# Performance work log

Hardware: AMD Instinct MI355X
Metric: run time of the kernel (lower is better)

The kernel has to match this reference:

```python
import jax, jax.numpy as jnp
import numpy as np

N_NODE = 100000
N_EDGE = 1600000
IN_DIM = 128
HID = [64, 64]
OUT_DIM = 32
NUM_GRAPHS = 256


def setup_inputs() -> dict:
    key = jax.random.key(0)
    ks = jax.random.split(key, 12)
    x = jax.random.normal(ks[0], (N_NODE, IN_DIM), dtype=jnp.float32)
    senders = jax.random.randint(ks[1], (N_EDGE,), 0, N_NODE, dtype=jnp.int32)
    receivers = jax.random.randint(ks[2], (N_EDGE,), 0, N_NODE, dtype=jnp.int32)
    batch = jnp.sort(jax.random.randint(ks[3], (N_NODE,), 0, NUM_GRAPHS, dtype=jnp.int32))
    # Dense params for the 3 GCN layers (Glorot-ish scaling)
    def dense(k, din, dout):
        return jax.random.normal(k, (din, dout), dtype=jnp.float32) / np.sqrt(din)
    W1 = dense(ks[4], IN_DIM, HID[0]); b1 = jnp.zeros((HID[0],), jnp.float32)
    W2 = dense(ks[5], HID[0], HID[1]); b2 = jnp.zeros((HID[1],), jnp.float32)
    W3 = dense(ks[6], HID[1], OUT_DIM); b3 = jnp.zeros((OUT_DIM,), jnp.float32)
    return {"x": x, "W1": W1, "b1": b1, "W2": W2, "b2": b2, "W3": W3, "b3": b3,
            "senders": senders, "receivers": receivers, "batch": batch,
            "num_graphs": NUM_GRAPHS}


def _gcn_layer(x, W, b, senders, receivers, n_node):
    # Dense transform
    x = x @ W + b  # [N, dout]
    ones = jnp.ones(senders.shape[0], dtype=x.dtype)
    sender_deg = jax.ops.segment_sum(ones, senders, n_node)      # out-degree
    receiver_deg = jax.ops.segment_sum(ones, receivers, n_node)  # in-degree
    # symmetric normalization: D^{-1/2} A D^{-1/2}
    x = x * jax.lax.rsqrt(jnp.maximum(sender_deg, 1.0))[:, None]
    x = jax.ops.segment_sum(x[senders], receivers, n_node)       # gather + scatter-sum
    x = x * jax.lax.rsqrt(jnp.maximum(receiver_deg, 1.0))[:, None]
    return x


def reference(x, W1, b1, W2, b2, W3, b3, senders, receivers, batch, num_graphs):
    n_node = x.shape[0]
    x = jax.nn.relu(_gcn_layer(x, W1, b1, senders, receivers, n_node))
    x = jax.nn.relu(_gcn_layer(x, W2, b2, senders, receivers, n_node))
    x = _gcn_layer(x, W3, b3, senders, receivers, n_node)
    # graph-level sum pooling
    return jax.ops.segment_sum(x, batch, num_graphs)  # [num_graphs, OUT_DIM]
```

## Files before the change

### kernel.cpp

```cpp
#include <hip/hip_runtime.h>
#include <hip/hip_bf16.h>

#define N_NODE   100000
#define N_EDGE   1600000
#define IN_DIM   128
#define HID1     64
#define HID2     64
#define OUT_DIM  32
#define NUM_GRAPHS 256

#define NBUCK    782
#define BBLK     500
#define EPB      3200
#define STAGE_CAP 4096

typedef unsigned int uint;
typedef unsigned char uchar;
typedef unsigned short ushort_t;
typedef short bf16x8 __attribute__((ext_vector_type(8)));
typedef float f32x4 __attribute__((ext_vector_type(4)));

__device__ __forceinline__ float bflo(uint p) { return __uint_as_float(p << 16); }
__device__ __forceinline__ float bfhi(uint p) { return __uint_as_float(p & 0xFFFF0000u); }
__device__ __forceinline__ uint bfpack(float a, float b) {
    uint ua = __float_as_uint(a), ub = __float_as_uint(b);
    ua = (ua + 0x7FFFu + ((ua >> 16) & 1u)) >> 16;
    ub = (ub + 0x7FFFu + ((ub >> 16) & 1u)) & 0xFFFF0000u;
    return ua | ub;
}
__device__ __forceinline__ ushort_t bf16r(float f) {
    uint ua = __float_as_uint(f);
    return (ushort_t)((ua + 0x7FFFu + ((ua >> 16) & 1u)) >> 16);
}


__global__ __launch_bounds__(256)
void k_count(const int2* __restrict__ snd2, const int2* __restrict__ rcv2,
             int* __restrict__ cntRA, int* __restrict__ cntSA) {
    __shared__ int cntR[NBUCK];
    __shared__ int cntS[NBUCK];
    const int t = threadIdx.x, blk = blockIdx.x;
    for (int i = t; i < NBUCK; i += 256) { cntR[i] = 0; cntS[i] = 0; }
    __syncthreads();
    const int base2 = blk * (EPB / 2);
    for (int i = 0; i < 7; ++i) {
        int local2 = i * 256 + t;
        if (local2 < EPB / 2) {
            int2 r = rcv2[base2 + local2];
            int2 s = snd2[base2 + local2];
            atomicAdd(&cntR[r.x >> 7], 1);
            atomicAdd(&cntR[r.y >> 7], 1);
            atomicAdd(&cntS[s.x >> 7], 1);
            atomicAdd(&cntS[s.y >> 7], 1);
        }
    }
    __syncthreads();
    for (int i = t; i < NBUCK; i += 256) {
        cntRA[blk * NBUCK + i] = cntR[i];
        cntSA[blk * NBUCK + i] = cntS[i];
    }
}

__global__ __launch_bounds__(256)
void k_scanb(int* __restrict__ cntRA, int* __restrict__ cntSA,
             int* __restrict__ rTotal, int* __restrict__ sTotal) {
    const int which = blockIdx.x / NBUCK;
    const int b = blockIdx.x % NBUCK;
    int* cntA = which ? cntSA : cntRA;
    int* total = which ? sTotal : rTotal;
    const int t = threadIdx.x, lane = t & 63, wave = t >> 6;
    __shared__ int sW[4];
    int carry = 0;
    for (int k = 0; k < 2; ++k) {
        int idx = k * 256 + t;
        int v = (idx < BBLK) ? cntA[idx * NBUCK + b] : 0;
        int inc = v;
        #pragma unroll
        for (int o = 1; o < 64; o <<= 1) { int n = __shfl_up(inc, o); if (lane >= o) inc += n; }
        if (lane == 63) sW[wave] = inc;
        __syncthreads();
        int wOff = 0;
        for (int w = 0; w < wave; ++w) wOff += sW[w];
        int tot = sW[0] + sW[1] + sW[2] + sW[3];
        int excl = carry + wOff + inc - v;
        if (idx < BBLK) cntA[idx * NBUCK + b] = excl;
        carry += tot;
        __syncthreads();
    }
    if (t == 0) total[b] = carry;
}

__global__ __launch_bounds__(256)
void k_scanB(const int* __restrict__ rTotal, const int* __restrict__ sTotal,
             int* __restrict__ rBase, int* __restrict__ sBase) {
    const int* total = blockIdx.x ? sTotal : rTotal;
    int* base = blockIdx.x ? sBase : rBase;
    const int t = threadIdx.x, lane = t & 63, wave = t >> 6;
    __shared__ int sW[4];
    int carry = 0;
    for (int k = 0; k < 4; ++k) {
        int idx = k * 256 + t;
        int v = (idx < NBUCK) ? total[idx] : 0;
        int inc = v;
        #pragma unroll
        for (int o = 1; o < 64; o <<= 1) { int n = __shfl_up(inc, o); if (lane >= o) inc += n; }
        if (lane == 63) sW[wave] = inc;
        __syncthreads();
        int wOff = 0;
        for (int w = 0; w < wave; ++w) wOff += sW[w];
        int tot = sW[0] + sW[1] + sW[2] + sW[3];
        int excl = carry + wOff + inc - v;
        if (idx < NBUCK) base[idx] = excl;
        carry += tot;
        __syncthreads();
    }
    if (t == 0) base[NBUCK] = carry;
}

__global__ __launch_bounds__(256)
void k_place(const int2* __restrict__ snd2, const int2* __restrict__ rcv2,
             const int* __restrict__ rColOff, const int* __restrict__ sColOff,
             const int* __restrict__ rBase, const int* __restrict__ sBase,
             uint* __restrict__ binned, uchar* __restrict__ sBin) {
    __shared__ int curR[NBUCK];
    __shared__ int curS[NBUCK];
    const int t = threadIdx.x, blk = blockIdx.x;
    for (int i = t; i < NBUCK; i += 256) { curR[i] = 0; curS[i] = 0; }
    __syncthreads();
    const int base2 = blk * (EPB / 2);
    for (int i = 0; i < 7; ++i) {
        int local2 = i * 256 + t;
        if (local2 < EPB / 2) {
            int2 r = rcv2[base2 + local2];
            int2 s = snd2[base2 + local2];
            int b0 = r.x >> 7, b1 = r.y >> 7;
            int l0 = atomicAdd(&curR[b0], 1);
            binned[rBase[b0] + rColOff[blk * NBUCK + b0] + l0] = ((uint)s.x << 7) | (uint)(r.x & 127);
            int l1 = atomicAdd(&curR[b1], 1);
            binned[rBase[b1] + rColOff[blk * NBUCK + b1] + l1] = ((uint)s.y << 7) | (uint)(r.y & 127);
            int c0 = s.x >> 7, c1 = s.y >> 7;
            int m0 = atomicAdd(&curS[c0], 1);
            sBin[sBase[c0] + sColOff[blk * NBUCK + c0] + m0] = (uchar)(s.x & 127);
            int m1 = atomicAdd(&curS[c1], 1);
            sBin[sBase[c1] + sColOff[blk * NBUCK + c1] + m1] = (uchar)(s.y & 127);
        }
    }
}

__global__ __launch_bounds__(256)
void k_local(const uint* __restrict__ binned, const uchar* __restrict__ sBin,
             const int* __restrict__ rBase, const int* __restrict__ sBase,
             int* __restrict__ rowptr, float* __restrict__ normS, float* __restrict__ normR,
             int* __restrict__ sortedSrc) {
    __shared__ uint staged[STAGE_CAP];
    __shared__ int cnt[128], excl[128], cur[128], cntS2[128];
    const int b = blockIdx.x, t = threadIdx.x;
    const int e0 = rBase[b], e1 = rBase[b + 1], m = e1 - e0;
    const int s0 = sBase[b], s1 = sBase[b + 1], ms = s1 - s0;
    if (t < 128) { cnt[t] = 0; cur[t] = 0; cntS2[t] = 0; }
    __syncthreads();
    for (int i = t; i < m; i += 256) {
        uint v = binned[e0 + i];
        if (i < STAGE_CAP) staged[i] = v;
        atomicAdd(&cnt[v & 127u], 1);
    }
    for (int i = t; i < ms; i += 256) {
        atomicAdd(&cntS2[(int)sBin[s0 + i]], 1);
    }
    __syncthreads();
    if (t < 64) {
        int v0 = cnt[t], v1 = cnt[64 + t];
        int i0 = v0;
        #pragma unroll
        for (int o = 1; o < 64; o <<= 1) { int n = __shfl_up(i0, o); if (t >= o) i0 += n; }
        excl[t] = i0 - v0;
        int tot0 = __shfl(i0, 63);
        int i1 = v1;
        #pragma unroll
        for (int o = 1; o < 64; o <<= 1) { int n = __shfl_up(i1, o); if (t >= o) i1 += n; }
        excl[64 + t] = tot0 + i1 - v1;
    }
    __syncthreads();
    if (t < 128) {
        int node = b * 128 + t;
        if (node < N_NODE) {
            rowptr[node] = e0 + excl[t];
            normR[node] = rsqrtf(fmaxf((float)cnt[t], 1.0f));
            normS[node] = rsqrtf(fmaxf((float)cntS2[t], 1.0f));
        }
    }
    if (b == NBUCK - 1 && t == 0) rowptr[N_NODE] = e1;
    for (int i = t; i < m; i += 256) {
        uint v = (i < STAGE_CAP) ? staged[i] : binned[e0 + i];
        int n7 = (int)(v & 127u);
        int lpos = atomicAdd(&cur[n7], 1);
        sortedSrc[e0 + excl[n7] + lpos] = (int)(v >> 7);
    }
}


__global__ __launch_bounds__(256)
void k_prepw(const float* __restrict__ W1, const float* __restrict__ W2,
             const float* __restrict__ W3,
             ushort_t* __restrict__ Wt1, ushort_t* __restrict__ Wt2,
             ushort_t* __restrict__ Wt3) {
    int i = blockIdx.x * 256 + threadIdx.x;
    if (i < 8192) {
        int col = i >> 7, k = i & 127;
        Wt1[i] = bf16r(W1[k * 64 + col]);
    } else if (i < 12288) {
        int j = i - 8192; int col = j >> 6, k = j & 63;
        Wt2[j] = bf16r(W2[k * 64 + col]);
    } else if (i < 14336) {
        int j = i - 12288; int col = j >> 6, k = j & 63;
        Wt3[j] = bf16r(W3[k * 32 + col]);
    }
}


template<int K, int N, bool F32IN>
__global__ __launch_bounds__(256)
void k_mgemm(const void* __restrict__ Xv, const ushort_t* __restrict__ Wt,
             const float* __restrict__ bias, const float* __restrict__ normS,
             uint* __restrict__ Y2) {
    __shared__ uint WL[N * K / 2];
    const int tid = threadIdx.x, wave = tid >> 6, lane = tid & 63;
    const uint* Wg = (const uint*)Wt;
    for (int i = tid; i < N * K / 2; i += 256) {
        int col = i / (K / 2);
        WL[i ^ ((col & 7) << 2)] = Wg[i];
    }
    const int m0 = blockIdx.x * 64 + wave * 16;
    const int arow = m0 + (lane & 15);
    const int asrc = (arow < N_NODE) ? arow : 0;
    const int koff = (lane >> 4) * 8;
    bf16x8 afr[K / 32];
    if (F32IN) {
        const float* Xf = (const float*)Xv + (size_t)asrc * K + koff;
        #pragma unroll
        for (int s = 0; s < K / 32; ++s) {
            float4 u = *(const float4*)(Xf + 32 * s);
            float4 v = *(const float4*)(Xf + 32 * s + 4);
            union { uint u4[4]; bf16x8 v8; } c;
            c.u4[0] = bfpack(u.x, u.y); c.u4[1] = bfpack(u.z, u.w);
            c.u4[2] = bfpack(v.x, v.y); c.u4[3] = bfpack(v.z, v.w);
            afr[s] = c.v8;
        }
    } else {
        const uint* Xp = (const uint*)Xv + (size_t)asrc * (K / 2) + (koff >> 1);
        #pragma unroll
        for (int s = 0; s < K / 32; ++s) {
            uint2 q0 = *(const uint2*)(Xp + 16 * s);
            uint2 q1 = *(const uint2*)(Xp + 16 * s + 2);
            union { uint u4[4]; bf16x8 v8; } c;
            c.u4[0] = q0.x; c.u4[1] = q0.y; c.u4[2] = q1.x; c.u4[3] = q1.y;
            afr[s] = c.v8;
        }
    }
    __syncthreads();
    f32x4 acc[N / 16];
    #pragma unroll
    for (int t = 0; t < N / 16; ++t) acc[t] = (f32x4){0.f, 0.f, 0.f, 0.f};
    #pragma unroll
    for (int s = 0; s < K / 32; ++s) {
        #pragma unroll
        for (int t = 0; t < N / 16; ++t) {
            int col = t * 16 + (lane & 15);
            int word = (col * (K / 2) + s * 16 + (koff >> 1)) ^ ((col & 7) << 2);
            bf16x8 bfr = *(const bf16x8*)&WL[word];
            acc[t] = __builtin_amdgcn_mfma_f32_16x16x32_bf16(afr[s], bfr, acc[t], 0, 0, 0);
        }
    }
    const int r0 = m0 + (lane >> 4) * 4;
    float ns[4];
    #pragma unroll
    for (int i = 0; i < 4; ++i) ns[i] = (r0 + i < N_NODE) ? normS[r0 + i] : 0.f;
    #pragma unroll
    for (int t = 0; t < N / 16; ++t) {
        int col = t * 16 + (lane & 15);
        float bv = bias[col];
        #pragma unroll
        for (int i = 0; i < 4; ++i) {
            float v = (acc[t][i] + bv) * ns[i];
            float w = __shfl_down(v, 1);
            if ((lane & 1) == 0 && r0 + i < N_NODE)
                Y2[(size_t)(r0 + i) * (N / 2) + (col >> 1)] = bfpack(v, w);
        }
    }
}


template<int F, bool RELU>
__global__ __launch_bounds__(256)
void k_agg(const uint* __restrict__ H2, const int* __restrict__ rowptr,
           const int* __restrict__ srcs, const float* __restrict__ normR,
           uint* __restrict__ Y2) {
    const int node = (blockIdx.x * 256 + threadIdx.x) >> 6;
    const int lane = threadIdx.x & 63;
    const int F2 = F / 2;
    const int PE = 64 / F2;
    const int sub = lane / F2;
    const int fj = lane % F2;
    const int start = rowptr[node], end = rowptr[node + 1];
    float a0 = 0.0f, a1 = 0.0f;
    int e = start + sub;
    for (; e + 3 * PE < end; e += 4 * PE) {
        int s0 = srcs[e], s1 = srcs[e + PE], s2 = srcs[e + 2 * PE], s3 = srcs[e + 3 * PE];
        uint p0 = H2[s0 * F2 + fj];
        uint p1 = H2[s1 * F2 + fj];
        uint p2 = H2[s2 * F2 + fj];
        uint p3 = H2[s3 * F2 + fj];
        a0 += bflo(p0); a1 += bfhi(p0);
        a0 += bflo(p1); a1 += bfhi(p1);
        a0 += bflo(p2); a1 += bfhi(p2);
        a0 += bflo(p3); a1 += bfhi(p3);
    }
    for (; e < end; e += PE) {
        uint p = H2[srcs[e] * F2 + fj];
        a0 += bflo(p); a1 += bfhi(p);
    }
    if (PE == 4) { a0 += __shfl_xor(a0, 16); a1 += __shfl_xor(a1, 16); }
    a0 += __shfl_xor(a0, 32); a1 += __shfl_xor(a1, 32);
    if (lane < F2) {
        float nr = normR[node];
        float r0 = a0 * nr, r1 = a1 * nr;
        if (RELU) { r0 = fmaxf(r0, 0.0f); r1 = fmaxf(r1, 0.0f); }
        Y2[node * F2 + fj] = bfpack(r0, r1);
    }
}


__global__ __launch_bounds__(256)
void k_pool(const uint* __restrict__ H2, const int* __restrict__ batch,
            float* __restrict__ out) {
    const int wid = (blockIdx.x * 256 + threadIdx.x) >> 6;
    const int lane = threadIdx.x & 63;
    const int NPW = (N_NODE + 1023) / 1024;
    int n0 = wid * NPW, n1 = min(n0 + NPW, N_NODE);
    const int p = lane >> 4, fj = lane & 15;
    float a0 = 0.0f, a1 = 0.0f;
    int gCur = -1;
    for (int n = n0 + p; n < n1; n += 4) {
        int g = batch[n];
        uint v = H2[n * 16 + fj];
        if (g != gCur) {
            if (gCur >= 0) {
                atomicAdd(&out[gCur * OUT_DIM + 2 * fj], a0);
                atomicAdd(&out[gCur * OUT_DIM + 2 * fj + 1], a1);
            }
            gCur = g; a0 = bflo(v); a1 = bfhi(v);
        } else {
            a0 += bflo(v); a1 += bfhi(v);
        }
    }
    if (gCur >= 0) {
        atomicAdd(&out[gCur * OUT_DIM + 2 * fj], a0);
        atomicAdd(&out[gCur * OUT_DIM + 2 * fj + 1], a1);
    }
}


extern "C" void kernel_launch(void* const* d_in, const int* in_sizes, int n_in,
                              void* d_out, int out_size, void* d_ws, size_t ws_size,
                              hipStream_t stream) {
    const float* x   = (const float*)d_in[0];
    const float* W1  = (const float*)d_in[1];
    const float* b1  = (const float*)d_in[2];
    const float* W2  = (const float*)d_in[3];
    const float* b2  = (const float*)d_in[4];
    const float* W3  = (const float*)d_in[5];
    const float* b3  = (const float*)d_in[6];
    const int* snd   = (const int*)d_in[7];
    const int* rcv   = (const int*)d_in[8];
    const int* batch = (const int*)d_in[9];
    float* out = (float*)d_out;

    char* ws = (char*)d_ws;
    size_t off = 0;
    auto carve = [&](size_t bytes) { char* p = ws + off; off += (bytes + 15) & ~size_t(15); return p; };
    int*   cntRA       = (int*)  carve((size_t)BBLK * NBUCK * 4);
    int*   cntSA       = (int*)  carve((size_t)BBLK * NBUCK * 4);
    int*   rTotal      = (int*)  carve(NBUCK * 4);
    int*   sTotal      = (int*)  carve(NBUCK * 4);
    int*   rBase       = (int*)  carve((NBUCK + 1) * 4);
    int*   sBase       = (int*)  carve((NBUCK + 1) * 4);
    int*   rowptr      = (int*)  carve((N_NODE + 1) * 4);
    uint*  binned      = (uint*) carve((size_t)N_EDGE * 4);
    uchar* sBin        = (uchar*)carve((size_t)N_EDGE);
    int*   sortedSrc   = (int*)  carve((size_t)N_EDGE * 4);
    float* normS       = (float*)carve(N_NODE * 4);
    float* normR       = (float*)carve(N_NODE * 4);
    ushort_t* Wt1      = (ushort_t*)carve(8192 * 2);
    ushort_t* Wt2      = (ushort_t*)carve(4096 * 2);
    ushort_t* Wt3      = (ushort_t*)carve(2048 * 2);
    uint*  bufA        = (uint*) carve((size_t)N_NODE * 32 * 4);
    uint*  bufB        = (uint*) carve((size_t)N_NODE * 32 * 4);

    hipMemsetAsync(d_out, 0, NUM_GRAPHS * OUT_DIM * 4, stream);

    k_prepw<<<56, 256, 0, stream>>>(W1, W2, W3, Wt1, Wt2, Wt3);
    k_count<<<BBLK, 256, 0, stream>>>((const int2*)snd, (const int2*)rcv, cntRA, cntSA);
    k_scanb<<<2 * NBUCK, 256, 0, stream>>>(cntRA, cntSA, rTotal, sTotal);
    k_scanB<<<2, 256, 0, stream>>>(rTotal, sTotal, rBase, sBase);
    k_place<<<BBLK, 256, 0, stream>>>((const int2*)snd, (const int2*)rcv, cntRA, cntSA,
                                      rBase, sBase, binned, sBin);
    k_local<<<NBUCK, 256, 0, stream>>>(binned, sBin, rBase, sBase,
                                       rowptr, normS, normR, sortedSrc);

    const int AGG_B = (N_NODE * 64 + 255) / 256;
    const int GB = (N_NODE + 63) / 64;

    k_mgemm<IN_DIM, HID1, true><<<GB, 256, 0, stream>>>(x, Wt1, b1, normS, bufA);
    k_agg<HID1, true><<<AGG_B, 256, 0, stream>>>(bufA, rowptr, sortedSrc, normR, bufB);

    k_mgemm<HID1, HID2, false><<<GB, 256, 0, stream>>>(bufB, Wt2, b2, normS, bufA);
    k_agg<HID2, true><<<AGG_B, 256, 0, stream>>>(bufA, rowptr, sortedSrc, normR, bufB);

    k_mgemm<HID2, OUT_DIM, false><<<GB, 256, 0, stream>>>(bufB, Wt3, b3, normS, bufA);
    k_agg<OUT_DIM, false><<<AGG_B, 256, 0, stream>>>(bufA, rowptr, sortedSrc, normR, bufB);

    k_pool<<<256, 256, 0, stream>>>(bufB, batch, out);
}
```

Measured before the change: 380.1 us.

## Split layer-1 aggregation into feature slices and vectorize layer-2 gather

Layer-1 aggregation now runs as four launches, each gathering a 16-feature slice (32 bytes per neighbour row) so that each pass's random-gather working set is a quarter of the feature table. Layer-2 aggregation uses a new kernel where 16 lanes each load a uint2 (four bf16) per neighbour, four neighbours are processed in parallel per wave, and the loop is unrolled by four. The slicing is meant to improve L2 hit rates on the random sender gathers. In exchange the CSR index array is read four times, there are extra launches, and each gather moves only 32 bytes.

Measured after the change: 470.7 us. 23.8% more time.

```diff
diff --git a/kernel.cpp b/kernel.cpp
--- a/kernel.cpp
+++ b/kernel.cpp
@@ -289,6 +289,77 @@
     }
 }
 
+
+template<int F2, int SLICE_U, bool RELU>
+__global__ __launch_bounds__(256)
+void k_agg_slice(const uint* __restrict__ H2, const int* __restrict__ rowptr,
+                 const int* __restrict__ srcs, const float* __restrict__ normR,
+                 uint* __restrict__ Y2, int off0) {
+    const int node = (blockIdx.x * 256 + threadIdx.x) >> 6;
+    const int lane = threadIdx.x & 63;
+    const int LPE = SLICE_U / 2;
+    const int PE  = 64 / LPE;
+    const int p = lane / LPE, q = lane % LPE;
+    const int start = rowptr[node], end = rowptr[node + 1];
+    float a0 = 0.f, a1 = 0.f, a2 = 0.f, a3 = 0.f;
+    for (int e = start + p; e < end; e += PE) {
+        int s = srcs[e];
+        uint2 v = *(const uint2*)&H2[(size_t)s * F2 + off0 + q * 2];
+        a0 += bflo(v.x); a1 += bfhi(v.x);
+        a2 += bflo(v.y); a3 += bfhi(v.y);
+    }
+    #pragma unroll
+    for (int m = LPE; m < 64; m <<= 1) {
+        a0 += __shfl_xor(a0, m); a1 += __shfl_xor(a1, m);
+        a2 += __shfl_xor(a2, m); a3 += __shfl_xor(a3, m);
+    }
+    if (lane < LPE) {
+        float nr = normR[node];
+        a0 *= nr; a1 *= nr; a2 *= nr; a3 *= nr;
+        if (RELU) { a0 = fmaxf(a0, 0.f); a1 = fmaxf(a1, 0.f); a2 = fmaxf(a2, 0.f); a3 = fmaxf(a3, 0.f); }
+        *(uint2*)&Y2[(size_t)node * F2 + off0 + q * 2] = make_uint2(bfpack(a0, a1), bfpack(a2, a3));
+    }
+}
+
+template<bool RELU>
+__global__ __launch_bounds__(256)
+void k_agg64v(const uint* __restrict__ H2, const int* __restrict__ rowptr,
+              const int* __restrict__ srcs, const float* __restrict__ normR,
+              uint* __restrict__ Y2) {
+    const int node = (blockIdx.x * 256 + threadIdx.x) >> 6;
+    const int lane = threadIdx.x & 63;
+    const int p = lane >> 4;
+    const int q = lane & 15;
+    const int start = rowptr[node], end = rowptr[node + 1];
+    float a0 = 0.f, a1 = 0.f, a2 = 0.f, a3 = 0.f;
+    int e = start + p;
+    for (; e + 12 < end; e += 16) {
+        int s0 = srcs[e], s1 = srcs[e + 4], s2 = srcs[e + 8], s3 = srcs[e + 12];
+        uint2 v0 = *(const uint2*)&H2[(size_t)s0 * 32 + q * 2];
+        uint2 v1 = *(const uint2*)&H2[(size_t)s1 * 32 + q * 2];
+        uint2 v2 = *(const uint2*)&H2[(size_t)s2 * 32 + q * 2];
+        uint2 v3 = *(const uint2*)&H2[(size_t)s3 * 32 + q * 2];
+        a0 += bflo(v0.x); a1 += bfhi(v0.x); a2 += bflo(v0.y); a3 += bfhi(v0.y);
+        a0 += bflo(v1.x); a1 += bfhi(v1.x); a2 += bflo(v1.y); a3 += bfhi(v1.y);
+        a0 += bflo(v2.x); a1 += bfhi(v2.x); a2 += bflo(v2.y); a3 += bfhi(v2.y);
+        a0 += bflo(v3.x); a1 += bfhi(v3.x); a2 += bflo(v3.y); a3 += bfhi(v3.y);
+    }
+    for (; e < end; e += 4) {
+        int s = srcs[e];
+        uint2 v = *(const uint2*)&H2[(size_t)s * 32 + q * 2];
+        a0 += bflo(v.x); a1 += bfhi(v.x); a2 += bflo(v.y); a3 += bfhi(v.y);
+    }
+    a0 += __shfl_xor(a0, 16); a1 += __shfl_xor(a1, 16);
+    a2 += __shfl_xor(a2, 16); a3 += __shfl_xor(a3, 16);
+    a0 += __shfl_xor(a0, 32); a1 += __shfl_xor(a1, 32);
+    a2 += __shfl_xor(a2, 32); a3 += __shfl_xor(a3, 32);
+    if (lane < 16) {
+        float nr = normR[node];
+        a0 *= nr; a1 *= nr; a2 *= nr; a3 *= nr;
+        if (RELU) { a0 = fmaxf(a0, 0.f); a1 = fmaxf(a1, 0.f); a2 = fmaxf(a2, 0.f); a3 = fmaxf(a3, 0.f); }
+        *(uint2*)&Y2[(size_t)node * 32 + q * 2] = make_uint2(bfpack(a0, a1), bfpack(a2, a3));
+    }
+}
 
 template<int F, bool RELU>
 __global__ __launch_bounds__(256)
@@ -411,10 +482,13 @@
     const int GB = (N_NODE + 63) / 64;
 
     k_mgemm<IN_DIM, HID1, true><<<GB, 256, 0, stream>>>(x, Wt1, b1, normS, bufA);
-    k_agg<HID1, true><<<AGG_B, 256, 0, stream>>>(bufA, rowptr, sortedSrc, normR, bufB);
+    k_agg_slice<32, 8, true><<<AGG_B, 256, 0, stream>>>(bufA, rowptr, sortedSrc, normR, bufB, 0);
+    k_agg_slice<32, 8, true><<<AGG_B, 256, 0, stream>>>(bufA, rowptr, sortedSrc, normR, bufB, 8);
+    k_agg_slice<32, 8, true><<<AGG_B, 256, 0, stream>>>(bufA, rowptr, sortedSrc, normR, bufB, 16);
+    k_agg_slice<32, 8, true><<<AGG_B, 256, 0, stream>>>(bufA, rowptr, sortedSrc, normR, bufB, 24);
 
     k_mgemm<HID1, HID2, false><<<GB, 256, 0, stream>>>(bufB, Wt2, b2, normS, bufA);
-    k_agg<HID2, true><<<AGG_B, 256, 0, stream>>>(bufA, rowptr, sortedSrc, normR, bufB);
+    k_agg64v<true><<<AGG_B, 256, 0, stream>>>(bufA, rowptr, sortedSrc, normR, bufB);
 
     k_mgemm<HID2, OUT_DIM, false><<<GB, 256, 0, stream>>>(bufB, Wt3, b3, normS, bufA);
     k_agg<OUT_DIM, false><<<AGG_B, 256, 0, stream>>>(bufA, rowptr, sortedSrc, normR, bufB);
```
